# Kernel optimization log

Hardware: AMD Instinct MI355X
Metric: run time of the kernel (lower is better)

The kernel has to match this reference:

```python
import jax, jax.numpy as jnp
import numpy as np

# Model hyper-parameters (from CMRET __init__ defaults)
N_A, F, H, K, NK, L = 4096, 128, 4, 15, 50, 6
CUTOFF, TEMP, BOX, N_Z = 5.0, 2.0, 40.0, 100
DH = F // H  # per-head dim


def setup_inputs() -> dict:
    key = jax.random.key(0)
    ks = jax.random.split(key, 12)
    Z = jax.random.randint(ks[0], (1, N_A), 0, N_Z)
    R = jax.random.uniform(ks[1], (1, N_A, 3), dtype=jnp.float32) * BOX
    batch = jnp.ones((1, N_A, 1), jnp.float32)
    g = lambda k, shp, s: jax.random.normal(k, shp, jnp.float32) * s
    emb = g(ks[2], (N_Z, F), 1.0)
    Wq = g(ks[3], (L, F, F), F ** -0.5)
    Wk = g(ks[4], (L, F, F), F ** -0.5)
    Wv = g(ks[5], (L, F, 3 * F), F ** -0.5)
    We_k = g(ks[6], (L, NK, F), NK ** -0.5)
    be_k = jnp.zeros((L, F), jnp.float32)
    We_v = g(ks[7], (L, NK, 3 * F), NK ** -0.5)
    be_v = jnp.zeros((L, 3 * F), jnp.float32)
    ln_g = jnp.ones((F,), jnp.float32)
    ln_b = jnp.zeros((F,), jnp.float32)
    Wo1 = g(ks[8], (F, F), F ** -0.5)
    Wo2 = g(ks[9], (F, 1), F ** -0.5)
    return dict(Z=Z, R=R, batch=batch, emb=emb, Wq=Wq, Wk=Wk, Wv=Wv,
                We_k=We_k, be_k=be_k, We_v=We_v, be_v=be_v,
                ln_g=ln_g, ln_b=ln_b, Wo1=Wo1, Wo2=Wo2)


def reference(Z, R, batch, emb, Wq, Wk, Wv, We_k, be_k, We_v, be_v, ln_g, ln_b, Wo1, Wo2):
    n_a = Z.shape[1]
    r = R[0]                                  # (n_a, 3)
    b = batch[..., 0]                         # (1, n_a)
    bm = (b.T @ b) == 0                       # (n_a, n_a) cross-molecule mask
    # --- Distance: k-nearest-neighbour selection (gather-based) ---
    sq = jnp.sum(r * r, -1)
    d2 = sq[:, None] + sq[None, :] - 2.0 * (r @ r.T)
    d2 = jnp.where(bm | jnp.eye(n_a, dtype=bool), 1e9, jnp.maximum(d2, 0.0))
    _, idxs = jax.lax.top_k(-d2, K)           # (n_a, K) neighbour indices
    vec = r[idxs] - r[:, None, :]             # (n_a, K, 3)
    d = jnp.sqrt(jnp.sum(vec * vec, -1) + 1e-12)
    vec_norm = vec / d[..., None]
    # --- Gaussian RBF * cosine cutoff edge features ---
    mu = jnp.linspace(0.0, CUTOFF, NK, dtype=jnp.float32)
    delta = CUTOFF / NK
    cut = 0.5 * (jnp.cos(jnp.pi * d / CUTOFF) + 1.0) * (d <= CUTOFF)
    e = jnp.exp(-((d[..., None] - mu) ** 2) / (2.0 * delta * delta)) * cut[..., None]
    # --- embedding and channel init ---
    s = emb[Z[0]]                             # (n_a, F) scalar channel
    o = jnp.zeros_like(s)                     # residual accumulator
    v = jnp.zeros((n_a, 3, F), s.dtype)       # vector channel
    scale = jnp.asarray(1.0 / np.sqrt(DH * TEMP), jnp.float32)
    # --- attention interaction stack ---
    for l in range(L):
        q = (s @ Wq[l]).reshape(n_a, H, DH)
        kk = s @ Wk[l]
        val = s @ Wv[l]                       # (n_a, 3F)
        ek = jax.nn.silu(e @ We_k[l] + be_k[l])   # (n_a, K, F) edge key filter
        ev = jax.nn.silu(e @ We_v[l] + be_v[l])   # (n_a, K, 3F) edge value filter
        kh = (kk[idxs] * ek).reshape(n_a, K, H, DH)
        logits = jnp.einsum('nhd,nkhd->nkh', q, kh) * scale
        attn = jax.nn.softmax(logits, axis=1) * cut[..., None]
        wf = jnp.repeat(attn, DH, axis=-1)        # (n_a, K, F) per-channel weights
        m1, m2, m3 = jnp.split(val[idxs] * ev, 3, axis=-1)
        ds = jnp.sum(wf * m1, axis=1)             # scalar message (n_a, F)
        dv = jnp.sum((wf * m2)[:, :, None, :] * vec_norm[..., None]
                     + (wf * m3)[:, :, None, :] * v[idxs], axis=1)
        s = s + ds
        o = o + ds
        v = v + dv
    # --- final LayerNorm + readout ---
    mean = o.mean(-1, keepdims=True)
    var = o.var(-1, keepdims=True)
    o = (o - mean) / jnp.sqrt(var + 1e-5) * ln_g + ln_b
    h = jax.nn.silu(o @ Wo1) @ Wo2            # (n_a, 1) per-atom contribution
    return jnp.sum(h * batch[0], axis=0, keepdims=True)  # (1, 1) energy
```

## Files before the change

### kernel.cpp

```cpp
#include <hip/hip_runtime.h>
#include <math.h>

#define NATOMS 4096
#define FDIM   128
#define NHEAD  4
#define DHEAD  32
#define KNBR   15
#define NKER   50
#define NLAYER 6
#define QKVW   640

typedef __attribute__((ext_vector_type(8))) short short8;
typedef __attribute__((ext_vector_type(4))) float f32x4;

__device__ __forceinline__ float silu_f(float x) { return x / (1.0f + __expf(-x)); }

__device__ __forceinline__ unsigned long long shfl_xor_u64(unsigned long long v, int m) {
    unsigned lo = (unsigned)v, hi = (unsigned)(v >> 32);
    lo = (unsigned)__shfl_xor((int)lo, m);
    hi = (unsigned)__shfl_xor((int)hi, m);
    return ((unsigned long long)hi << 32) | lo;
}
__device__ __forceinline__ unsigned long long min_u64(unsigned long long a, unsigned long long b) {
    return a < b ? a : b;
}

__global__ __launch_bounds__(256) void knn_kernel(
    const float* __restrict__ R, const float* __restrict__ batch,
    int* __restrict__ idxs, float* __restrict__ cutw,
    float* __restrict__ vecn, float* __restrict__ ebuf)
{
    __shared__ float d2s[NATOMS];
    __shared__ unsigned long long wred[2][4];
    __shared__ int sel[KNBR];
    const int i = blockIdx.x, t = threadIdx.x;
    const int wave = t >> 6, lane = t & 63;
    const float xi = R[i*3+0], yi = R[i*3+1], zi = R[i*3+2];
    const float bi = batch[i];
    const float sqi = xi*xi + yi*yi + zi*zi;
    for (int j = t; j < NATOMS; j += 256) {
        float xj = R[j*3+0], yj = R[j*3+1], zj = R[j*3+2];
        float sqj = xj*xj + yj*yj + zj*zj;
        float d2 = sqi + sqj - 2.0f*(xi*xj + yi*yj + zi*zj);
        if (bi*batch[j] == 0.0f || j == i) d2 = 1e9f;
        else d2 = fmaxf(d2, 0.0f);
        d2s[j] = d2;
    }
    __syncthreads();

    unsigned long long cand = ~0ull;
    #pragma unroll
    for (int it = 0; it < 16; ++it) {
        int j = t + it*256;
        unsigned long long p = ((unsigned long long)__float_as_uint(d2s[j]) << 32) | (unsigned)j;
        cand = min_u64(cand, p);
    }
    for (int k = 0; k < KNBR; ++k) {
        unsigned long long w = cand;
        #pragma unroll
        for (int off = 1; off < 64; off <<= 1)
            w = min_u64(w, shfl_xor_u64(w, off));
        if (lane == 0) wred[k & 1][wave] = w;
        __syncthreads();
        unsigned long long f = min_u64(min_u64(wred[k&1][0], wred[k&1][1]),
                                       min_u64(wred[k&1][2], wred[k&1][3]));
        int sj = (int)(unsigned)f;
        if (t == 0) sel[k] = sj;
        if ((sj & 255) == t) {
            d2s[sj] = 1e9f;
            cand = ~0ull;
            #pragma unroll
            for (int it = 0; it < 16; ++it) {
                int j = t + it*256;
                unsigned long long p = ((unsigned long long)__float_as_uint(d2s[j]) << 32) | (unsigned)j;
                cand = min_u64(cand, p);
            }
        }
    }
    __syncthreads();

    if (t < KNBR) {
        int j = sel[t];
        idxs[i*KNBR + t] = j;
        float vx = R[j*3+0]-xi, vy = R[j*3+1]-yi, vz = R[j*3+2]-zi;
        float d = sqrtf(vx*vx + vy*vy + vz*vz + 1e-12f);
        float inv = 1.0f/d;
        vecn[(i*KNBR+t)*3+0] = vx*inv;
        vecn[(i*KNBR+t)*3+1] = vy*inv;
        vecn[(i*KNBR+t)*3+2] = vz*inv;
        const float PI = 3.14159265358979323846f;
        float cutv = (d <= 5.0f) ? 0.5f*(cosf(PI*d*0.2f) + 1.0f) : 0.0f;
        cutw[i*KNBR + t] = cutv;
        for (int jj = 0; jj < NKER; ++jj) {
            float mu = 5.0f * (float)jj / 49.0f;
            float dd = d - mu;
            ebuf[(i*KNBR+t)*NKER + jj] = __expf(-dd*dd*50.0f) * cutv;
        }
    }
}

__global__ __launch_bounds__(256) void init_kernel(
    const int* __restrict__ Z, const float* __restrict__ emb,
    float* __restrict__ s, float* __restrict__ o, float* __restrict__ v0)
{
    int stride = gridDim.x * blockDim.x;
    for (int idx = blockIdx.x*blockDim.x + threadIdx.x; idx < NATOMS*3*FDIM; idx += stride) {
        v0[idx] = 0.0f;
        if (idx < NATOMS*FDIM) {
            int a = idx >> 7, c = idx & 127;
            s[idx] = emb[Z[a]*FDIM + c];
            o[idx] = 0.0f;
        }
    }
}

__global__ __launch_bounds__(64) void wprep_kernel(
    const float* __restrict__ WeK, const float* __restrict__ WeV,
    unsigned short* __restrict__ Wswz)
{
    const int blk = blockIdx.x;
    const int lane = threadIdx.x;
    const int ks = blk & 1;
    const int T  = (blk >> 1) & 31;
    const int l  = blk >> 6;
    const int quad = lane >> 4, x = lane & 15;
    unsigned short* dst = Wswz + (size_t)blk*1024 + lane*8;
    for (int j = 0; j < 8; ++j) {
        int k = ks*32 + quad*8 + j;
        float w = 0.0f;
        if (k < NKER)
            w = (T < 8) ? WeK[l*NKER*FDIM + k*FDIM + T*16 + x]
                        : WeV[(size_t)l*NKER*3*FDIM + k*3*FDIM + (T-8)*16 + x];
        unsigned b = __float_as_uint(w);
        dst[j] = (unsigned short)(b >> 16);
        float r = w - __uint_as_float(b & 0xFFFF0000u);
        dst[512 + j] = (unsigned short)(__float_as_uint(r) >> 16);
    }
}

__global__ __launch_bounds__(64) void qprep_kernel(
    const float* __restrict__ Wq, const float* __restrict__ Wk,
    const float* __restrict__ Wv, unsigned short* __restrict__ Qswz)
{
    const int blk = blockIdx.x;
    const int lane = threadIdx.x;
    const int ks = blk & 3;
    const int ct = (blk >> 2) % 40;
    const int l  = blk / 160;
    const int quad = lane >> 4, lx = lane & 15;
    const int col = ct*16 + lx;
    unsigned short* dst = Qswz + (size_t)blk*1024 + lane*8;
    for (int j = 0; j < 8; ++j) {
        int k = ks*32 + quad*8 + j;
        float w;
        if (col < 128)      w = Wq[l*16384 + k*128 + col];
        else if (col < 256) w = Wk[l*16384 + k*128 + (col-128)];
        else                w = Wv[(size_t)l*49152 + k*384 + (col-256)];
        unsigned b = __float_as_uint(w);
        dst[j] = (unsigned short)(b >> 16);
        float r = w - __uint_as_float(b & 0xFFFF0000u);
        dst[512 + j] = (unsigned short)(__float_as_uint(r) >> 16);
    }
}

__global__ __launch_bounds__(128) void proj_kernel(
    const float* __restrict__ S, const unsigned short* __restrict__ Qswz,
    float* __restrict__ QKV, int l)
{
    const int rt = blockIdx.x;
    const int t = threadIdx.x, wave = t >> 6, lane = t & 63;
    const int quad = lane >> 4, lx = lane & 15;
    const int cg = blockIdx.y*2 + wave;

    short8 ah[4], al[4];
    const float* srow = S + (size_t)(rt*16 + lx)*FDIM;
    #pragma unroll
    for (int ks = 0; ks < 4; ++ks) {
        float v[8];
        *(f32x4*)&v[0] = *(const f32x4*)(srow + ks*32 + quad*8);
        *(f32x4*)&v[4] = *(const f32x4*)(srow + ks*32 + quad*8 + 4);
        #pragma unroll
        for (int j = 0; j < 8; ++j) {
            unsigned b = __float_as_uint(v[j]);
            ah[ks][j] = (short)(b >> 16);
            float r = v[j] - __uint_as_float(b & 0xFFFF0000u);
            al[ks][j] = (short)(__float_as_uint(r) >> 16);
        }
    }
    for (int ci = 0; ci < 10; ++ci) {
        const int ct = cg*10 + ci;
        const unsigned short* wp = Qswz + (size_t)((l*40 + ct)*4)*1024 + lane*8;
        f32x4 acc = {0.0f, 0.0f, 0.0f, 0.0f};
        #pragma unroll
        for (int ks = 0; ks < 4; ++ks) {
            short8 bh = *(const short8*)(wp + ks*1024);
            short8 bl = *(const short8*)(wp + ks*1024 + 512);
            acc = __builtin_amdgcn_mfma_f32_16x16x32_bf16(ah[ks], bh, acc, 0, 0, 0);
            acc = __builtin_amdgcn_mfma_f32_16x16x32_bf16(ah[ks], bl, acc, 0, 0, 0);
            acc = __builtin_amdgcn_mfma_f32_16x16x32_bf16(al[ks], bh, acc, 0, 0, 0);
        }
        const int col = ct*16 + lx;
        #pragma unroll
        for (int r = 0; r < 4; ++r)
            QKV[(size_t)(rt*16 + quad*4 + r)*QKVW + col] = acc[r];
    }
}

__global__ __launch_bounds__(512) void attn_kernel(
    const float* __restrict__ QKV, const int* __restrict__ idxs,
    const float* __restrict__ cutw, const float* __restrict__ vecn,
    const float* __restrict__ ebuf, const unsigned short* __restrict__ Wswz,
    const float* __restrict__ beK, const float* __restrict__ beV,
    float* __restrict__ s, float* __restrict__ o,
    const float* __restrict__ vin, float* __restrict__ vout, int l)
{
    __shared__ __align__(16) float es[16][68];
    __shared__ __align__(16) float fbuf[KNBR][516];
    __shared__ int   nidx[KNBR];
    __shared__ float cutv[KNBR];
    __shared__ float vnc[KNBR][3];
    __shared__ float attns[KNBR][NHEAD];
    __shared__ float dvbuf[3][FDIM];

    const int i = blockIdx.x, t = threadIdx.x;
    const int wave = t >> 6, lane = t & 63;
    const int quad = lane >> 4, lx = lane & 15;

    if (t < KNBR) {
        nidx[t] = idxs[i*KNBR + t];
        cutv[t] = cutw[i*KNBR + t];
        vnc[t][0] = vecn[(i*KNBR+t)*3+0];
        vnc[t][1] = vecn[(i*KNBR+t)*3+1];
        vnc[t][2] = vecn[(i*KNBR+t)*3+2];
    }
    for (int x = t; x < 16*64; x += 512) {
        int row = x >> 6, col = x & 63;
        es[row][col] = (row < KNBR && col < NKER)
                       ? ebuf[(size_t)i*KNBR*NKER + row*NKER + col] : 0.0f;
    }
    __syncthreads();

    for (int x = t; x < KNBR*128; x += 512) {
        int k = x >> 7, c4 = x & 127;
        *(f32x4*)&fbuf[k][c4*4] =
            *(const f32x4*)(QKV + (size_t)nidx[k]*QKVW + FDIM + c4*4);
    }

    short8 eh[2], el[2];
    #pragma unroll
    for (int ks = 0; ks < 2; ++ks) {
        float v[8];
        *(f32x4*)&v[0] = *(const f32x4*)&es[lx][ks*32 + quad*8];
        *(f32x4*)&v[4] = *(const f32x4*)&es[lx][ks*32 + quad*8 + 4];
        #pragma unroll
        for (int j = 0; j < 8; ++j) {
            unsigned b = __float_as_uint(v[j]);
            eh[ks][j] = (short)(b >> 16);
            float r = v[j] - __uint_as_float(b & 0xFFFF0000u);
            el[ks][j] = (short)(__float_as_uint(r) >> 16);
        }
    }
    __syncthreads();

    #pragma unroll
    for (int tt = 0; tt < 4; ++tt) {
        const int T = wave*4 + tt;
        const int col = T*16 + lx;
        f32x4 acc = {0.0f, 0.0f, 0.0f, 0.0f};
        #pragma unroll
        for (int ks = 0; ks < 2; ++ks) {
            const unsigned short* wp = Wswz + ((size_t)((l*32+T)*2+ks))*1024 + lane*8;
            short8 bh = *(const short8*)wp;
            short8 bl = *(const short8*)(wp + 512);
            acc = __builtin_amdgcn_mfma_f32_16x16x32_bf16(eh[ks], bh, acc, 0, 0, 0);
            acc = __builtin_amdgcn_mfma_f32_16x16x32_bf16(eh[ks], bl, acc, 0, 0, 0);
            acc = __builtin_amdgcn_mfma_f32_16x16x32_bf16(el[ks], bh, acc, 0, 0, 0);
        }
        const float b = (col < FDIM) ? beK[l*FDIM + col]
                                     : beV[(size_t)l*3*FDIM + (col - FDIM)];
        #pragma unroll
        for (int r = 0; r < 4; ++r) {
            int k = quad*4 + r;
            if (k < KNBR) {
                float f = silu_f(acc[r] + b);
                fbuf[k][col] = f * fbuf[k][col];
            }
        }
    }
    __syncthreads();

    if (t < FDIM) {
        const int c = t, h = c >> 5;
        const float q = QKV[(size_t)i*QKVW + c];
        float lg[KNBR];
        #pragma unroll
        for (int k = 0; k < KNBR; ++k) {
            float p = q * fbuf[k][c];
            p += __shfl_xor(p, 1);
            p += __shfl_xor(p, 2);
            p += __shfl_xor(p, 4);
            p += __shfl_xor(p, 8);
            p += __shfl_xor(p, 16);
            lg[k] = p * 0.125f;
        }
        float m = -1e30f;
        #pragma unroll
        for (int k = 0; k < KNBR; ++k) m = fmaxf(m, lg[k]);
        float ssum = 0.0f;
        #pragma unroll
        for (int k = 0; k < KNBR; ++k) { lg[k] = __expf(lg[k]-m); ssum += lg[k]; }
        float inv = 1.0f/ssum;
        if ((c & 31) == 0) {
            #pragma unroll
            for (int k = 0; k < KNBR; ++k) attns[k][h] = lg[k]*inv*cutv[k];
        }
    }
    float mval[KNBR];
    int cv = 0, h2 = 0;
    if (t >= FDIM) {
        cv = t - FDIM; h2 = (cv & 127) >> 5;
        #pragma unroll
        for (int k = 0; k < KNBR; ++k) mval[k] = fbuf[k][FDIM + cv];
    }
    __syncthreads();

    if (t >= FDIM) {
        if (cv < FDIM) {
            float ds = 0.0f;
            #pragma unroll
            for (int k = 0; k < KNBR; ++k) ds += attns[k][h2]*mval[k];
            s[i*FDIM + cv] += ds;
            o[i*FDIM + cv] += ds;
        } else if (cv < 2*FDIM) {
            const int cc = cv - FDIM;
            float d0 = 0.0f, d1 = 0.0f, d2 = 0.0f;
            #pragma unroll
            for (int k = 0; k < KNBR; ++k) {
                float w = attns[k][h2]*mval[k];
                d0 += w*vnc[k][0]; d1 += w*vnc[k][1]; d2 += w*vnc[k][2];
            }
            dvbuf[0][cc] = d0; dvbuf[1][cc] = d1; dvbuf[2][cc] = d2;
        }
    }
    float d3[3] = {0.0f, 0.0f, 0.0f};
    if (t >= FDIM && cv >= 2*FDIM) {
        const int cc = cv - 2*FDIM;
        #pragma unroll
        for (int k = 0; k < KNBR; ++k) {
            float w = attns[k][h2]*mval[k];
            const float* vb = vin + (size_t)nidx[k]*3*FDIM + cc;
            d3[0] += w*vb[0*FDIM]; d3[1] += w*vb[1*FDIM]; d3[2] += w*vb[2*FDIM];
        }
    }
    __syncthreads();
    if (t >= FDIM && cv >= 2*FDIM) {
        const int cc = cv - 2*FDIM;
        #pragma unroll
        for (int x = 0; x < 3; ++x) {
            size_t off = (size_t)i*3*FDIM + x*FDIM + cc;
            vout[off] = vin[off] + dvbuf[x][cc] + d3[x];
        }
    }
}

__global__ __launch_bounds__(128) void final_kernel(
    const float* __restrict__ o, const float* __restrict__ lng, const float* __restrict__ lnb,
    const float* __restrict__ Wo1, const float* __restrict__ Wo2,
    const float* __restrict__ batch, float* __restrict__ hout)
{
    __shared__ float red[128];
    __shared__ float on[128];
    const int i = blockIdx.x, t = threadIdx.x;
    float x = o[i*FDIM + t];
    red[t] = x; __syncthreads();
    for (int off = 64; off > 0; off >>= 1) { if (t < off) red[t] += red[t+off]; __syncthreads(); }
    float mean = red[0] * (1.0f/128.0f);
    __syncthreads();
    float xm = x - mean;
    red[t] = xm*xm; __syncthreads();
    for (int off = 64; off > 0; off >>= 1) { if (t < off) red[t] += red[t+off]; __syncthreads(); }
    float var = red[0] * (1.0f/128.0f);
    __syncthreads();
    on[t] = xm * rsqrtf(var + 1e-5f) * lng[t] + lnb[t];
    __syncthreads();
    float acc = 0.0f;
    #pragma unroll 8
    for (int j = 0; j < 128; ++j) acc += on[j] * Wo1[j*128 + t];
    float h = silu_f(acc) * Wo2[t];
    red[t] = h; __syncthreads();
    for (int off = 64; off > 0; off >>= 1) { if (t < off) red[t] += red[t+off]; __syncthreads(); }
    if (t == 0) hout[i] = red[0] * batch[i];
}

__global__ __launch_bounds__(1024) void reduce_kernel(
    const float* __restrict__ hout, float* __restrict__ out)
{
    __shared__ float red[1024];
    const int t = threadIdx.x;
    float a = hout[t] + hout[t+1024] + hout[t+2048] + hout[t+3072];
    red[t] = a; __syncthreads();
    for (int off = 512; off > 0; off >>= 1) {
        if (t < off) red[t] += red[t+off];
        __syncthreads();
    }
    if (t == 0) out[0] = red[0];
}

extern "C" void kernel_launch(void* const* d_in, const int* in_sizes, int n_in,
                              void* d_out, int out_size, void* d_ws, size_t ws_size,
                              hipStream_t stream)
{
    const int*   Z     = (const int*)  d_in[0];
    const float* R     = (const float*)d_in[1];
    const float* batch = (const float*)d_in[2];
    const float* emb   = (const float*)d_in[3];
    const float* Wq    = (const float*)d_in[4];
    const float* Wk    = (const float*)d_in[5];
    const float* Wv    = (const float*)d_in[6];
    const float* WeK   = (const float*)d_in[7];
    const float* beK   = (const float*)d_in[8];
    const float* WeV   = (const float*)d_in[9];
    const float* beV   = (const float*)d_in[10];
    const float* lng   = (const float*)d_in[11];
    const float* lnb   = (const float*)d_in[12];
    const float* Wo1   = (const float*)d_in[13];
    const float* Wo2   = (const float*)d_in[14];
    float* out = (float*)d_out;

    float* fws = (float*)d_ws;
    float* s    = fws; fws += NATOMS*FDIM;
    float* o    = fws; fws += NATOMS*FDIM;
    float* v0   = fws; fws += NATOMS*3*FDIM;
    float* v1   = fws; fws += NATOMS*3*FDIM;
    float* qkv  = fws; fws += NATOMS*QKVW;
    float* cutw = fws; fws += NATOMS*KNBR;
    float* vecn = fws; fws += NATOMS*KNBR*3;
    float* ebuf = fws; fws += NATOMS*KNBR*NKER;
    float* hout = fws; fws += NATOMS;
    int*   idxs = (int*)fws; fws += NATOMS*KNBR;
    unsigned short* Wswz = (unsigned short*)fws;
    fws += (NLAYER*32*2*1024) / 2;
    unsigned short* Qswz = (unsigned short*)fws;

    wprep_kernel<<<NLAYER*32*2, 64, 0, stream>>>(WeK, WeV, Wswz);
    qprep_kernel<<<NLAYER*40*4, 64, 0, stream>>>(Wq, Wk, Wv, Qswz);
    knn_kernel<<<NATOMS, 256, 0, stream>>>(R, batch, idxs, cutw, vecn, ebuf);
    init_kernel<<<1024, 256, 0, stream>>>(Z, emb, s, o, v0);
    for (int l = 0; l < NLAYER; ++l) {
        proj_kernel<<<dim3(256, 2), 128, 0, stream>>>(s, Qswz, qkv, l);
        float* vin  = (l & 1) ? v1 : v0;
        float* vout = (l & 1) ? v0 : v1;
        attn_kernel<<<NATOMS, 512, 0, stream>>>(qkv, idxs, cutw, vecn, ebuf, Wswz,
                                                beK, beV, s, o, vin, vout, l);
    }
    final_kernel<<<NATOMS, 128, 0, stream>>>(o, lng, lnb, Wo1, Wo2, batch, hout);
    reduce_kernel<<<1, 1024, 0, stream>>>(hout, out);
}
```

Measured before the change: 587.8 us.

## Reorder atoms along a Morton curve to improve neighbour-gather locality

Adds a single-block counting-sort kernel that assigns each atom a 12-bit Morton code from its position and builds perm/rank arrays. All per-atom buffers (s, o, v, idxs, edge features) are then stored in Morton order, and neighbour indices are remapped through rank. Spatially close atoms now sit close in memory, so the per-layer gathers of neighbour k/v and vector features should hit cache more often. The cost is an extra serial one-block kernel with a 1024-step-log scan, plus one indirection in the knn, init and final kernels.

```diff
diff --git a/kernel.cpp b/kernel.cpp
--- a/kernel.cpp
+++ b/kernel.cpp
@@ -24,16 +24,68 @@
 __device__ __forceinline__ unsigned long long min_u64(unsigned long long a, unsigned long long b) {
     return a < b ? a : b;
 }
+__device__ __forceinline__ int spread3(int v) {
+    return (v & 1) | ((v & 2) << 2) | ((v & 4) << 4) | ((v & 8) << 6);
+}
+
+__global__ __launch_bounds__(1024) void morton_kernel(
+    const float* __restrict__ R, int* __restrict__ perm, int* __restrict__ rank)
+{
+    __shared__ int hist[4096];
+    __shared__ int tscan[1024];
+    const int t = threadIdx.x;
+    int codes[4];
+    #pragma unroll
+    for (int u = 0; u < 4; ++u) hist[t*4 + u] = 0;
+    __syncthreads();
+    #pragma unroll
+    for (int u = 0; u < 4; ++u) {
+        int i = t + u*1024;
+        float x = R[i*3+0], y = R[i*3+1], z = R[i*3+2];
+        int cx = min(15, max(0, (int)(x * (16.0f/40.0f))));
+        int cy = min(15, max(0, (int)(y * (16.0f/40.0f))));
+        int cz = min(15, max(0, (int)(z * (16.0f/40.0f))));
+        int code = spread3(cx) | (spread3(cy) << 1) | (spread3(cz) << 2);
+        codes[u] = code;
+        atomicAdd(&hist[code], 1);
+    }
+    __syncthreads();
+    int loc[4], s0 = 0;
+    #pragma unroll
+    for (int u = 0; u < 4; ++u) { loc[u] = hist[t*4 + u]; s0 += loc[u]; }
+    tscan[t] = s0;
+    __syncthreads();
+    for (int off = 1; off < 1024; off <<= 1) {
+        int v = tscan[t];
+        int a = (t >= off) ? tscan[t - off] : 0;
+        __syncthreads();
+        tscan[t] = v + a;
+        __syncthreads();
+    }
+    int run = tscan[t] - s0;
+    #pragma unroll
+    for (int u = 0; u < 4; ++u) { hist[t*4 + u] = run; run += loc[u]; }
+    __syncthreads();
+    #pragma unroll
+    for (int u = 0; u < 4; ++u) {
+        int i = t + u*1024;
+        int r = atomicAdd(&hist[codes[u]], 1);
+        perm[r] = i;
+        rank[i] = r;
+    }
+}
 
 __global__ __launch_bounds__(256) void knn_kernel(
     const float* __restrict__ R, const float* __restrict__ batch,
+    const int* __restrict__ perm, const int* __restrict__ rank,
     int* __restrict__ idxs, float* __restrict__ cutw,
     float* __restrict__ vecn, float* __restrict__ ebuf)
 {
     __shared__ float d2s[NATOMS];
     __shared__ unsigned long long wred[2][4];
     __shared__ int sel[KNBR];
-    const int i = blockIdx.x, t = threadIdx.x;
+    const int r = blockIdx.x, t = threadIdx.x;
+    const int i = perm[r];
     const int wave = t >> 6, lane = t & 63;
     const float xi = R[i*3+0], yi = R[i*3+1], zi = R[i*3+2];
     const float bi = batch[i];
@@ -81,26 +133,27 @@
 
     if (t < KNBR) {
         int j = sel[t];
-        idxs[i*KNBR + t] = j;
+        idxs[r*KNBR + t] = rank[j];
         float vx = R[j*3+0]-xi, vy = R[j*3+1]-yi, vz = R[j*3+2]-zi;
         float d = sqrtf(vx*vx + vy*vy + vz*vz + 1e-12f);
         float inv = 1.0f/d;
-        vecn[(i*KNBR+t)*3+0] = vx*inv;
-        vecn[(i*KNBR+t)*3+1] = vy*inv;
-        vecn[(i*KNBR+t)*3+2] = vz*inv;
+        vecn[(r*KNBR+t)*3+0] = vx*inv;
+        vecn[(r*KNBR+t)*3+1] = vy*inv;
+        vecn[(r*KNBR+t)*3+2] = vz*inv;
         const float PI = 3.14159265358979323846f;
         float cutv = (d <= 5.0f) ? 0.5f*(cosf(PI*d*0.2f) + 1.0f) : 0.0f;
-        cutw[i*KNBR + t] = cutv;
+        cutw[r*KNBR + t] = cutv;
         for (int jj = 0; jj < NKER; ++jj) {
             float mu = 5.0f * (float)jj / 49.0f;
             float dd = d - mu;
-            ebuf[(i*KNBR+t)*NKER + jj] = __expf(-dd*dd*50.0f) * cutv;
+            ebuf[(r*KNBR+t)*NKER + jj] = __expf(-dd*dd*50.0f) * cutv;
         }
     }
 }
 
 __global__ __launch_bounds__(256) void init_kernel(
     const int* __restrict__ Z, const float* __restrict__ emb,
+    const int* __restrict__ perm,
     float* __restrict__ s, float* __restrict__ o, float* __restrict__ v0)
 {
     int stride = gridDim.x * blockDim.x;
@@ -108,7 +161,7 @@
         v0[idx] = 0.0f;
         if (idx < NATOMS*FDIM) {
             int a = idx >> 7, c = idx & 127;
-            s[idx] = emb[Z[a]*FDIM + c];
+            s[idx] = emb[Z[perm[a]]*FDIM + c];
             o[idx] = 0.0f;
         }
     }
@@ -366,7 +419,8 @@
 __global__ __launch_bounds__(128) void final_kernel(
     const float* __restrict__ o, const float* __restrict__ lng, const float* __restrict__ lnb,
     const float* __restrict__ Wo1, const float* __restrict__ Wo2,
-    const float* __restrict__ batch, float* __restrict__ hout)
+    const float* __restrict__ batch, const int* __restrict__ perm,
+    float* __restrict__ hout)
 {
     __shared__ float red[128];
     __shared__ float on[128];
@@ -389,7 +443,7 @@
     float h = silu_f(acc) * Wo2[t];
     red[t] = h; __syncthreads();
     for (int off = 64; off > 0; off >>= 1) { if (t < off) red[t] += red[t+off]; __syncthreads(); }
-    if (t == 0) hout[i] = red[0] * batch[i];
+    if (t == 0) hout[i] = red[0] * batch[perm[i]];
 }
 
 __global__ __launch_bounds__(1024) void reduce_kernel(
@@ -438,14 +492,17 @@
     float* ebuf = fws; fws += NATOMS*KNBR*NKER;
     float* hout = fws; fws += NATOMS;
     int*   idxs = (int*)fws; fws += NATOMS*KNBR;
+    int*   perm = (int*)fws; fws += NATOMS;
+    int*   rank = (int*)fws; fws += NATOMS;
     unsigned short* Wswz = (unsigned short*)fws;
     fws += (NLAYER*32*2*1024) / 2;
     unsigned short* Qswz = (unsigned short*)fws;
 
+    morton_kernel<<<1, 1024, 0, stream>>>(R, perm, rank);
     wprep_kernel<<<NLAYER*32*2, 64, 0, stream>>>(WeK, WeV, Wswz);
     qprep_kernel<<<NLAYER*40*4, 64, 0, stream>>>(Wq, Wk, Wv, Qswz);
-    knn_kernel<<<NATOMS, 256, 0, stream>>>(R, batch, idxs, cutw, vecn, ebuf);
-    init_kernel<<<1024, 256, 0, stream>>>(Z, emb, s, o, v0);
+    knn_kernel<<<NATOMS, 256, 0, stream>>>(R, batch, perm, rank, idxs, cutw, vecn, ebuf);
+    init_kernel<<<1024, 256, 0, stream>>>(Z, emb, perm, s, o, v0);
     for (int l = 0; l < NLAYER; ++l) {
         proj_kernel<<<dim3(256, 2), 128, 0, stream>>>(s, Qswz, qkv, l);
         float* vin  = (l & 1) ? v1 : v0;
@@ -453,6 +510,6 @@
         attn_kernel<<<NATOMS, 512, 0, stream>>>(qkv, idxs, cutw, vecn, ebuf, Wswz,
                                                 beK, beV, s, o, vin, vout, l);
     }
-    final_kernel<<<NATOMS, 128, 0, stream>>>(o, lng, lnb, Wo1, Wo2, batch, hout);
+    final_kernel<<<NATOMS, 128, 0, stream>>>(o, lng, lnb, Wo1, Wo2, batch, perm, hout);
     reduce_kernel<<<1, 1024, 0, stream>>>(hout, out);
 }
```

Result: faster. 571.3 us (-2.8%).
